# Kernel tuning notes

Measured on AMD Instinct MI355X. Metric: run time of the kernel, lower is better.

## Reference

```python
import jax, jax.numpy as jnp
import numpy as np

SPATIAL_SCALE = 0.125  # stride-8 FPN level
POINTS = 5


def _sample_points(bb):
    # bb: [N,H,W,5] = (cx, cy, w, h, theta) in image coords
    cx, cy, w, h, t = [bb[..., i] for i in range(5)]
    if POINTS == 1:
        px = cx[..., None]
        py = cy[..., None]
    else:
        vx = w * jnp.cos(t) * 0.5
        vy = w * jnp.sin(t) * 0.5
        wx = -h * jnp.sin(t) * 0.5
        wy = h * jnp.cos(t) * 0.5
        px = jnp.stack([cx, cx + vx + wx, cx - vx + wx, cx - vx - wx, cx + vx - wx], axis=-1)
        py = jnp.stack([cy, cy + vy + wy, cy - vy + wy, cy - vy - wy, cy + vy - wy], axis=-1)
    return px * SPATIAL_SCALE, py * SPATIAL_SCALE  # [N,H,W,P] feature-map coords


def _bilinear_gather(feat, y, x):
    # feat: [N,C,H,W]; y,x: [N,H,W,P] -> [N,H,W,P,C], mmcv-style bilinear w/ border rules
    N, C, H, W = feat.shape
    valid = (y >= -1.0) & (y <= H) & (x >= -1.0) & (x <= W)
    y = jnp.maximum(y, 0.0)
    x = jnp.maximum(x, 0.0)
    y_low = jnp.minimum(jnp.floor(y).astype(jnp.int32), H - 1)
    x_low = jnp.minimum(jnp.floor(x).astype(jnp.int32), W - 1)
    # if low index hits last row/col, snap coordinate onto it (ly/lx = 0)
    y = jnp.where(y_low >= H - 1, y_low.astype(feat.dtype), y)
    x = jnp.where(x_low >= W - 1, x_low.astype(feat.dtype), x)
    y_high = jnp.minimum(y_low + 1, H - 1)
    x_high = jnp.minimum(x_low + 1, W - 1)
    ly = y - y_low.astype(feat.dtype)
    lx = x - x_low.astype(feat.dtype)
    hy = 1.0 - ly
    hx = 1.0 - lx
    nn = jnp.arange(N)[:, None, None, None]  # broadcasts against [N,H,W,P]

    def g(yy, xx):
        return feat[nn, :, yy, xx]  # [N,H,W,P,C]

    val = ((hy * hx)[..., None] * g(y_low, x_low)
           + (hy * lx)[..., None] * g(y_low, x_high)
           + (ly * hx)[..., None] * g(y_high, x_low)
           + (ly * lx)[..., None] * g(y_high, x_high))
    return jnp.where(valid[..., None], val, 0.0)


def feature_refine(features, best_rbboxes):
    px, py = _sample_points(best_rbboxes)
    sampled = _bilinear_gather(features, py, px)       # [N,H,W,P,C]
    acc = sampled.sum(axis=3)                           # [N,H,W,C]
    return features + jnp.transpose(acc, (0, 3, 1, 2))  # [N,C,H,W]


def setup_inputs() -> dict:
    key = jax.random.key(0)
    k1, k2, k3, k4, k5, k6 = jax.random.split(key, 6)
    N, C, H, W = 4, 256, 128, 128
    IMG = 1024.0
    features = jax.random.normal(k1, (N, C, H, W), dtype=jnp.float32)
    cx = jax.random.uniform(k2, (N, H, W), minval=0.0, maxval=IMG)
    cy = jax.random.uniform(k3, (N, H, W), minval=0.0, maxval=IMG)
    bw = jax.random.uniform(k4, (N, H, W), minval=8.0, maxval=128.0)
    bh = jax.random.uniform(k5, (N, H, W), minval=8.0, maxval=128.0)
    th = jax.random.uniform(k6, (N, H, W), minval=-np.pi / 2, maxval=np.pi / 2)
    best_rbboxes = jnp.stack([cx, cy, bw, bh, th], axis=-1)  # [N,H,W,5]
    return {"features": features, "best_rbboxes": best_rbboxes}


def reference(features, best_rbboxes):
    return feature_refine(features, best_rbboxes)
```

## Files before the change

### kernel.cpp

```cpp
#include <hip/hip_runtime.h>


#define N_ 4
#define C_ 256
#define H_ 128
#define W_ 128
#define HW_ (H_ * W_)
#define SCALE 0.125f

typedef unsigned int uint32;

__device__ __forceinline__ uint32 f2bf(float f) {
    uint32 u = __float_as_uint(f);
    u = (u + 0x7FFF + ((u >> 16) & 1)) >> 16;
    return u;
}
__device__ __forceinline__ float blo(uint32 u) { return __uint_as_float(u << 16); }
__device__ __forceinline__ float bhi(uint32 u) { return __uint_as_float(u & 0xFFFF0000u); }

__global__ __launch_bounds__(1024, 8) void nchw2nhwc_geo(const float* __restrict__ in,
                                                         const float* __restrict__ bb,
                                                         uint32* __restrict__ outU,
                                                         uint32* __restrict__ geoG)
{
    __shared__ uint32 tile[64 * 260];
    const int t   = threadIdx.x;
    const int l   = t & 63;
    const int g   = t >> 6;
    const int hw0 = blockIdx.x * 256;
    const int ch  = blockIdx.y;
    const int n   = blockIdx.z;

    if (ch == 0 && t < 256) {
        const int px = n * HW_ + hw0 + t;
        const float* b = bb + (size_t)px * 5;
        const float cx = b[0], cy = b[1], bw = b[2], bh = b[3], th = b[4];
        const float st = sinf(th), ct = cosf(th);
        const float vx = bw * ct * 0.5f, vy = bw * st * 0.5f;
        const float wx = -bh * st * 0.5f, wy = bh * ct * 0.5f;
        const float pxs[5] = {cx, cx + vx + wx, cx - vx + wx, cx - vx - wx, cx + vx - wx};
        const float pys[5] = {cy, cy + vy + wy, cy - vy + wy, cy - vy - wy, cy + vy - wy};
        uint32* gw = geoG + (size_t)px * 32;
#pragma unroll
        for (int p = 0; p < 5; ++p) {
            float x = pxs[p] * SCALE;
            float y = pys[p] * SCALE;
            const bool valid = (y >= -1.0f) && (y <= (float)H_) &&
                               (x >= -1.0f) && (x <= (float)W_);
            y = fmaxf(y, 0.0f);
            x = fmaxf(x, 0.0f);
            int yl = min((int)y, H_ - 1);
            int xl = min((int)x, W_ - 1);
            if (yl >= H_ - 1) y = (float)yl;
            if (xl >= W_ - 1) x = (float)xl;
            const int yh = min(yl + 1, H_ - 1);
            const float ly = y - (float)yl, lx = x - (float)xl;
            const float hy = 1.0f - ly,     hx = 1.0f - lx;
            const int xa = min(xl, W_ - 2);
            float wA, wB;
            if (xl < W_ - 1) { wA = hx; wB = lx; }
            else             { wA = 0.0f; wB = 1.0f; }
            const float v = valid ? 1.0f : 0.0f;
            gw[p]      = (uint32)(yl * W_ + xa);
            gw[5 + p]  = (uint32)(yh * W_ + xa);
            gw[10 + p] = __float_as_uint(v * hy * wA);
            gw[15 + p] = __float_as_uint(v * hy * wB);
            gw[20 + p] = __float_as_uint(v * ly * wA);
            gw[25 + p] = __float_as_uint(v * ly * wB);
        }
        gw[30] = 0u; gw[31] = 0u;
    }

    const float* base = in + (size_t)n * C_ * HW_ + (size_t)(ch * 128) * HW_ + hw0 + 4 * l;
    float4 v0[4], v1[4];
#pragma unroll
    for (int r = 0; r < 4; ++r) {
        const int cp = g * 4 + r;
        v0[r] = *(const float4*)(base + (size_t)(2 * cp) * HW_);
        v1[r] = *(const float4*)(base + (size_t)(2 * cp + 1) * HW_);
    }
#pragma unroll
    for (int r = 0; r < 4; ++r) {
        const int cp = g * 4 + r;
        uint4 u;
        u.x = f2bf(v0[r].x) | (f2bf(v1[r].x) << 16);
        u.y = f2bf(v0[r].y) | (f2bf(v1[r].y) << 16);
        u.z = f2bf(v0[r].z) | (f2bf(v1[r].z) << 16);
        u.w = f2bf(v0[r].w) | (f2bf(v1[r].w) << 16);
        *(uint4*)&tile[cp * 260 + 4 * l] = u;
    }
    __syncthreads();
    uint32* dst = outU + ((size_t)n * HW_ + hw0) * 128 + ch * 64;
#pragma unroll
    for (int it = 0; it < 16; ++it) {
        const int f   = it * 1024 + t;
        const int row = f >> 6;
        const int q   = f & 63;
        dst[(size_t)row * 128 + q] = tile[q * 260 + row];
    }
}

__global__ __launch_bounds__(256, 8) void fr_refine(const uint32* __restrict__ nhwcU,
                                                    const uint32* __restrict__ geoG,
                                                    float* __restrict__ out)
{
    __shared__ float tile[32 * 128];
    const int t  = threadIdx.x;
    const int l  = t & 63;
    const int wv = __builtin_amdgcn_readfirstlane(t >> 6);
    const int bx = blockIdx.x;
    const int xcd = bx & 7;
    const int n   = xcd >> 1;
    const int ch  = xcd & 1;
    const int s   = bx >> 3;
    const int h   = s >> 2;
    const int w0  = (s & 3) * 32;

    const int chB = ch << 8;
    const int laneb = ((l & 15) << 4) + (((l >> 4) & 1) << 9);
    const bool hi = (l >= 32);
    const bool b4 = ((l >> 4) & 1) != 0;
    const int hwb = h * W_ + w0 + wv * 8;
    const uint32* gb = geoG + ((size_t)n * HW_ + hwb) * 32;
    const char* plane = (const char*)(nhwcU + (size_t)n * HW_ * 128);

#pragma unroll 1
    for (int p = 0; p < 8; ++p) {
        const uint32* g = gb + p * 32;

        int o0b[5], o1b[5];
        float w00[5], w01[5], w10[5], w11[5];
#pragma unroll
        for (int q = 0; q < 5; ++q) {
            o0b[q] = (int)__builtin_amdgcn_readfirstlane(g[q])     * 512 + chB;
            o1b[q] = (int)__builtin_amdgcn_readfirstlane(g[5 + q]) * 512 + chB;
            w00[q] = __uint_as_float(__builtin_amdgcn_readfirstlane(g[10 + q]));
            w01[q] = __uint_as_float(__builtin_amdgcn_readfirstlane(g[15 + q]));
            w10[q] = __uint_as_float(__builtin_amdgcn_readfirstlane(g[20 + q]));
            w11[q] = __uint_as_float(__builtin_amdgcn_readfirstlane(g[25 + q]));
        }

        uint4 rid = make_uint4(0u, 0u, 0u, 0u);
        if (l < 16)
            rid = *(const uint4*)(plane + (size_t)(hwb + p) * 512 + chB + ((l & 15) << 4));
        uint4 r[5];
#pragma unroll
        for (int q = 0; q < 5; ++q) {
            const int vof = (hi ? o1b[q] : o0b[q]) + laneb;
            r[q] = *(const uint4*)(plane + vof);
        }
        __builtin_amdgcn_sched_barrier(0);

        float a[8];
        a[0] = blo(rid.x); a[1] = bhi(rid.x);
        a[2] = blo(rid.y); a[3] = bhi(rid.y);
        a[4] = blo(rid.z); a[5] = bhi(rid.z);
        a[6] = blo(rid.w); a[7] = bhi(rid.w);
#pragma unroll
        for (int q = 0; q < 5; ++q) {
            const float wq = hi ? (b4 ? w11[q] : w10[q]) : (b4 ? w01[q] : w00[q]);
            a[0] = fmaf(wq, blo(r[q].x), a[0]); a[1] = fmaf(wq, bhi(r[q].x), a[1]);
            a[2] = fmaf(wq, blo(r[q].y), a[2]); a[3] = fmaf(wq, bhi(r[q].y), a[3]);
            a[4] = fmaf(wq, blo(r[q].z), a[4]); a[5] = fmaf(wq, bhi(r[q].z), a[5]);
            a[6] = fmaf(wq, blo(r[q].w), a[6]); a[7] = fmaf(wq, bhi(r[q].w), a[7]);
        }
#pragma unroll
        for (int k = 0; k < 8; ++k) {
            a[k] += __shfl_xor(a[k], 16, 64);
            a[k] += __shfl_xor(a[k], 32, 64);
        }
        if (l < 16) {
            const int px  = wv * 8 + p;
            const int swz = (px & 7) << 2;
            float* base = &tile[px * 128];
            *(float4*)&base[(l * 8) ^ swz]     = make_float4(a[0], a[1], a[2], a[3]);
            *(float4*)&base[(l * 8 + 4) ^ swz] = make_float4(a[4], a[5], a[6], a[7]);
        }
    }
    __syncthreads();
    const size_t obase = (size_t)n * C_ * HW_ + (size_t)(ch * 128) * HW_ + h * W_ + w0;
#pragma unroll
    for (int it = 0; it < 16; ++it) {
        const int flat = it * 256 + t;
        const int px = flat & 31;
        const int c  = flat >> 5;
        out[obase + (size_t)c * HW_ + px] = tile[px * 128 + (c ^ ((px & 7) << 2))];
    }
}

__global__ __launch_bounds__(256) void fr_kernel(
    const float* __restrict__ feat,
    const float* __restrict__ bb,
    float* __restrict__ out)
{
    const int lane = threadIdx.x & 63;
    const int wave = threadIdx.x >> 6;
    const int tile = blockIdx.x;
    const int wt   = tile & 1;
    const int h    = (tile >> 1) & (H_ - 1);
    const int n    = tile >> 8;
    const int w    = wt * 64 + lane;
    const int cb   = blockIdx.y;

    const float* b = bb + (size_t)((n * H_ + h) * W_ + w) * 5;
    const float cx = b[0], cy = b[1], bw = b[2], bh = b[3], th = b[4];
    const float st = sinf(th), ct = cosf(th);
    const float vx = bw * ct * 0.5f, vy = bw * st * 0.5f;
    const float wx = -bh * st * 0.5f, wy = bh * ct * 0.5f;
    const float pxs[5] = {cx, cx + vx + wx, cx - vx + wx, cx - vx - wx, cx + vx - wx};
    const float pys[5] = {cy, cy + vy + wy, cy - vy + wy, cy - vy - wy, cy + vy - wy};

    int   off0[5], off1[5];
    float wgt[20];
#pragma unroll
    for (int p = 0; p < 5; ++p) {
        float x = pxs[p] * SCALE;
        float y = pys[p] * SCALE;
        const bool valid = (y >= -1.0f) && (y <= (float)H_) &&
                           (x >= -1.0f) && (x <= (float)W_);
        y = fmaxf(y, 0.0f);
        x = fmaxf(x, 0.0f);
        int yl = min((int)y, H_ - 1);
        int xl = min((int)x, W_ - 1);
        if (yl >= H_ - 1) y = (float)yl;
        if (xl >= W_ - 1) x = (float)xl;
        const int yh = min(yl + 1, H_ - 1);
        const float ly = y - (float)yl, lx = x - (float)xl;
        const float hy = 1.0f - ly,     hx = 1.0f - lx;
        const int xa = min(xl, W_ - 2);
        float wA, wB;
        if (xl < W_ - 1) { wA = hx; wB = lx; }
        else             { wA = 0.0f; wB = 1.0f; }
        const float v = valid ? 1.0f : 0.0f;
        off0[p] = yl * W_ + xa;
        off1[p] = yh * W_ + xa;
        wgt[p * 4 + 0] = v * hy * wA;
        wgt[p * 4 + 1] = v * hy * wB;
        wgt[p * 4 + 2] = v * ly * wA;
        wgt[p * 4 + 3] = v * ly * wB;
    }

    const int hw = h * W_ + w;
    const size_t planeBase = ((size_t)n * C_ + cb * 64 + wave * 16) * HW_;
    const float* fp = feat + planeBase;
    float*       op = out  + planeBase;
    for (int it = 0; it < 16; ++it) {
        float acc = fp[hw];
#pragma unroll
        for (int p = 0; p < 5; ++p) {
            acc += wgt[p * 4 + 0] * fp[off0[p]]
                 + wgt[p * 4 + 1] * fp[off0[p] + 1]
                 + wgt[p * 4 + 2] * fp[off1[p]]
                 + wgt[p * 4 + 3] * fp[off1[p] + 1];
        }
        op[hw] = acc;
        fp += HW_;
        op += HW_;
    }
}

extern "C" void kernel_launch(void* const* d_in, const int* in_sizes, int n_in,
                              void* d_out, int out_size, void* d_ws, size_t ws_size,
                              hipStream_t stream) {
    const float* feat = (const float*)d_in[0];
    const float* bbox = (const float*)d_in[1];
    float* out = (float*)d_out;

    const size_t nhwcBytes = (size_t)N_ * HW_ * C_ * 2;
    const size_t geoBytes  = (size_t)N_ * HW_ * 32 * 4;
    if (ws_size >= nhwcBytes + geoBytes) {
        uint32* nhwcU = (uint32*)d_ws;
        uint32* geoG  = (uint32*)((char*)d_ws + nhwcBytes);
        nchw2nhwc_geo<<<dim3(HW_ / 256, 2, N_), dim3(1024), 0, stream>>>(feat, bbox, nhwcU, geoG);
        fr_refine<<<dim3(N_ * H_ * (W_ / 32) * 2), dim3(256), 0, stream>>>(nhwcU, geoG, out);
    } else {
        dim3 grid(N_ * H_ * (W_ / 64), C_ / 64, 1);
        fr_kernel<<<grid, dim3(256), 0, stream>>>(feat, bbox, out);
    }
}
```

Baseline: 158.6 us.

## Shrink transpose blocks, batch scalar geo loads, packed FMA, fp32 residual add

The transpose kernel now uses 512-thread blocks, each covering 128 pixels, with a smaller LDS tile, which gives more blocks and better occupancy. Gather offsets are pre-scaled to bytes in the geometry buffer. The refine kernel loads each pixel's 32-word geometry record with two s_load_dwordx16 instructions instead of many readfirstlane loads, and it accumulates with v_pk_fma_f32. The identity term is no longer a bf16 gather: fp32 features are read and added at the output store. That improves accuracy but adds an extra fp32 read of the full feature tensor.

```diff
diff --git a/kernel.cpp b/kernel.cpp
--- a/kernel.cpp
+++ b/kernel.cpp
@@ -9,6 +9,8 @@
 #define SCALE 0.125f
 
 typedef unsigned int uint32;
+typedef uint32 u32x16 __attribute__((ext_vector_type(16)));
+typedef float  f32x2  __attribute__((ext_vector_type(2)));
 
 __device__ __forceinline__ uint32 f2bf(float f) {
     uint32 u = __float_as_uint(f);
@@ -18,20 +20,22 @@
 __device__ __forceinline__ float blo(uint32 u) { return __uint_as_float(u << 16); }
 __device__ __forceinline__ float bhi(uint32 u) { return __uint_as_float(u & 0xFFFF0000u); }
 
-__global__ __launch_bounds__(1024, 8) void nchw2nhwc_geo(const float* __restrict__ in,
-                                                         const float* __restrict__ bb,
-                                                         uint32* __restrict__ outU,
-                                                         uint32* __restrict__ geoG)
+__global__ __launch_bounds__(512, 8) void nchw2nhwc_geo(const float* __restrict__ in,
+                                                        const float* __restrict__ bb,
+                                                        uint32* __restrict__ outU,
+                                                        uint32* __restrict__ geoG)
 {
-    __shared__ uint32 tile[64 * 260];
+    __shared__ uint32 tile[64 * 132];
     const int t   = threadIdx.x;
     const int l   = t & 63;
     const int g   = t >> 6;
-    const int hw0 = blockIdx.x * 256;
+    const int lw  = l & 31;
+    const int half = l >> 5;
+    const int hw0 = blockIdx.x * 128;
     const int ch  = blockIdx.y;
     const int n   = blockIdx.z;
 
-    if (ch == 0 && t < 256) {
+    if (ch == 0 && t < 128) {
         const int px = n * HW_ + hw0 + t;
         const float* b = bb + (size_t)px * 5;
         const float cx = b[0], cy = b[1], bw = b[2], bh = b[3], th = b[4];
@@ -61,8 +65,8 @@
             if (xl < W_ - 1) { wA = hx; wB = lx; }
             else             { wA = 0.0f; wB = 1.0f; }
             const float v = valid ? 1.0f : 0.0f;
-            gw[p]      = (uint32)(yl * W_ + xa);
-            gw[5 + p]  = (uint32)(yh * W_ + xa);
+            gw[p]      = (uint32)((yl * W_ + xa) * 512);
+            gw[5 + p]  = (uint32)((yh * W_ + xa) * 512);
             gw[10 + p] = __float_as_uint(v * hy * wA);
             gw[15 + p] = __float_as_uint(v * hy * wB);
             gw[20 + p] = __float_as_uint(v * ly * wA);
@@ -71,37 +75,38 @@
         gw[30] = 0u; gw[31] = 0u;
     }
 
-    const float* base = in + (size_t)n * C_ * HW_ + (size_t)(ch * 128) * HW_ + hw0 + 4 * l;
+    const float* base = in + (size_t)n * C_ * HW_ + (size_t)(ch * 128) * HW_ + hw0 + 4 * lw;
     float4 v0[4], v1[4];
 #pragma unroll
     for (int r = 0; r < 4; ++r) {
-        const int cp = g * 4 + r;
+        const int cp = g * 8 + half * 4 + r;
         v0[r] = *(const float4*)(base + (size_t)(2 * cp) * HW_);
         v1[r] = *(const float4*)(base + (size_t)(2 * cp + 1) * HW_);
     }
 #pragma unroll
     for (int r = 0; r < 4; ++r) {
-        const int cp = g * 4 + r;
+        const int cp = g * 8 + half * 4 + r;
         uint4 u;
         u.x = f2bf(v0[r].x) | (f2bf(v1[r].x) << 16);
         u.y = f2bf(v0[r].y) | (f2bf(v1[r].y) << 16);
         u.z = f2bf(v0[r].z) | (f2bf(v1[r].z) << 16);
         u.w = f2bf(v0[r].w) | (f2bf(v1[r].w) << 16);
-        *(uint4*)&tile[cp * 260 + 4 * l] = u;
+        *(uint4*)&tile[cp * 132 + 4 * lw] = u;
     }
     __syncthreads();
     uint32* dst = outU + ((size_t)n * HW_ + hw0) * 128 + ch * 64;
 #pragma unroll
     for (int it = 0; it < 16; ++it) {
-        const int f   = it * 1024 + t;
+        const int f   = it * 512 + t;
         const int row = f >> 6;
         const int q   = f & 63;
-        dst[(size_t)row * 128 + q] = tile[q * 260 + row];
+        dst[(size_t)row * 128 + q] = tile[q * 132 + row];
     }
 }
 
 __global__ __launch_bounds__(256, 8) void fr_refine(const uint32* __restrict__ nhwcU,
                                                     const uint32* __restrict__ geoG,
+                                                    const float* __restrict__ feat,
                                                     float* __restrict__ out)
 {
     __shared__ float tile[32 * 128];
@@ -116,65 +121,67 @@
     const int h   = s >> 2;
     const int w0  = (s & 3) * 32;
 
-    const int chB = ch << 8;
     const int laneb = ((l & 15) << 4) + (((l >> 4) & 1) << 9);
     const bool hi = (l >= 32);
     const bool b4 = ((l >> 4) & 1) != 0;
     const int hwb = h * W_ + w0 + wv * 8;
     const uint32* gb = geoG + ((size_t)n * HW_ + hwb) * 32;
-    const char* plane = (const char*)(nhwcU + (size_t)n * HW_ * 128);
+    const char* plane = (const char*)(nhwcU + (size_t)n * HW_ * 128) + (ch << 8);
 
 #pragma unroll 1
     for (int p = 0; p < 8; ++p) {
         const uint32* g = gb + p * 32;
 
-        int o0b[5], o1b[5];
-        float w00[5], w01[5], w10[5], w11[5];
+        u32x16 S0, S1;
+        asm volatile("s_load_dwordx16 %0, %2, 0x0\n"
+                     "s_load_dwordx16 %1, %2, 0x40\n"
+                     "s_waitcnt lgkmcnt(0)\n"
+                     : "=&s"(S0), "=&s"(S1)
+                     : "s"(g));
+        __builtin_amdgcn_sched_barrier(0);
+#define GW(i) ((i) < 16 ? S0[(i)] : S1[(i) - 16])
+
+        uint4 r[5];
+        f32x2 w2[5];
 #pragma unroll
         for (int q = 0; q < 5; ++q) {
-            o0b[q] = (int)__builtin_amdgcn_readfirstlane(g[q])     * 512 + chB;
-            o1b[q] = (int)__builtin_amdgcn_readfirstlane(g[5 + q]) * 512 + chB;
-            w00[q] = __uint_as_float(__builtin_amdgcn_readfirstlane(g[10 + q]));
-            w01[q] = __uint_as_float(__builtin_amdgcn_readfirstlane(g[15 + q]));
-            w10[q] = __uint_as_float(__builtin_amdgcn_readfirstlane(g[20 + q]));
-            w11[q] = __uint_as_float(__builtin_amdgcn_readfirstlane(g[25 + q]));
-        }
-
-        uint4 rid = make_uint4(0u, 0u, 0u, 0u);
-        if (l < 16)
-            rid = *(const uint4*)(plane + (size_t)(hwb + p) * 512 + chB + ((l & 15) << 4));
-        uint4 r[5];
+            const int vof = (int)(hi ? GW(5 + q) : GW(q)) + laneb;
+            r[q] = *(const uint4*)(plane + vof);
+            const float wq = __uint_as_float(hi ? (b4 ? GW(25 + q) : GW(20 + q))
+                                                : (b4 ? GW(15 + q) : GW(10 + q)));
+            w2[q].x = wq; w2[q].y = wq;
+        }
+        __builtin_amdgcn_sched_barrier(0);
+#undef GW
+
+        f32x2 acc[4];
+#pragma unroll
+        for (int k = 0; k < 4; ++k) { acc[k].x = 0.0f; acc[k].y = 0.0f; }
 #pragma unroll
         for (int q = 0; q < 5; ++q) {
-            const int vof = (hi ? o1b[q] : o0b[q]) + laneb;
-            r[q] = *(const uint4*)(plane + vof);
-        }
-        __builtin_amdgcn_sched_barrier(0);
-
-        float a[8];
-        a[0] = blo(rid.x); a[1] = bhi(rid.x);
-        a[2] = blo(rid.y); a[3] = bhi(rid.y);
-        a[4] = blo(rid.z); a[5] = bhi(rid.z);
-        a[6] = blo(rid.w); a[7] = bhi(rid.w);
-#pragma unroll
-        for (int q = 0; q < 5; ++q) {
-            const float wq = hi ? (b4 ? w11[q] : w10[q]) : (b4 ? w01[q] : w00[q]);
-            a[0] = fmaf(wq, blo(r[q].x), a[0]); a[1] = fmaf(wq, bhi(r[q].x), a[1]);
-            a[2] = fmaf(wq, blo(r[q].y), a[2]); a[3] = fmaf(wq, bhi(r[q].y), a[3]);
-            a[4] = fmaf(wq, blo(r[q].z), a[4]); a[5] = fmaf(wq, bhi(r[q].z), a[5]);
-            a[6] = fmaf(wq, blo(r[q].w), a[6]); a[7] = fmaf(wq, bhi(r[q].w), a[7]);
-        }
-#pragma unroll
-        for (int k = 0; k < 8; ++k) {
-            a[k] += __shfl_xor(a[k], 16, 64);
-            a[k] += __shfl_xor(a[k], 32, 64);
+            f32x2 u0, u1, u2, u3;
+            u0.x = blo(r[q].x); u0.y = bhi(r[q].x);
+            u1.x = blo(r[q].y); u1.y = bhi(r[q].y);
+            u2.x = blo(r[q].z); u2.y = bhi(r[q].z);
+            u3.x = blo(r[q].w); u3.y = bhi(r[q].w);
+            asm("v_pk_fma_f32 %0, %1, %2, %0" : "+v"(acc[0]) : "v"(u0), "v"(w2[q]));
+            asm("v_pk_fma_f32 %0, %1, %2, %0" : "+v"(acc[1]) : "v"(u1), "v"(w2[q]));
+            asm("v_pk_fma_f32 %0, %1, %2, %0" : "+v"(acc[2]) : "v"(u2), "v"(w2[q]));
+            asm("v_pk_fma_f32 %0, %1, %2, %0" : "+v"(acc[3]) : "v"(u3), "v"(w2[q]));
+        }
+#pragma unroll
+        for (int k = 0; k < 4; ++k) {
+            acc[k].x += __shfl_xor(acc[k].x, 16, 64);
+            acc[k].y += __shfl_xor(acc[k].y, 16, 64);
+            acc[k].x += __shfl_xor(acc[k].x, 32, 64);
+            acc[k].y += __shfl_xor(acc[k].y, 32, 64);
         }
         if (l < 16) {
             const int px  = wv * 8 + p;
             const int swz = (px & 7) << 2;
             float* base = &tile[px * 128];
-            *(float4*)&base[(l * 8) ^ swz]     = make_float4(a[0], a[1], a[2], a[3]);
-            *(float4*)&base[(l * 8 + 4) ^ swz] = make_float4(a[4], a[5], a[6], a[7]);
+            *(float4*)&base[(l * 8) ^ swz]     = make_float4(acc[0].x, acc[0].y, acc[1].x, acc[1].y);
+            *(float4*)&base[(l * 8 + 4) ^ swz] = make_float4(acc[2].x, acc[2].y, acc[3].x, acc[3].y);
         }
     }
     __syncthreads();
@@ -184,7 +191,8 @@
         const int flat = it * 256 + t;
         const int px = flat & 31;
         const int c  = flat >> 5;
-        out[obase + (size_t)c * HW_ + px] = tile[px * 128 + (c ^ ((px & 7) << 2))];
+        const size_t idx = obase + (size_t)c * HW_ + px;
+        out[idx] = feat[idx] + tile[px * 128 + (c ^ ((px & 7) << 2))];
     }
 }
 
@@ -271,8 +279,8 @@
     if (ws_size >= nhwcBytes + geoBytes) {
         uint32* nhwcU = (uint32*)d_ws;
         uint32* geoG  = (uint32*)((char*)d_ws + nhwcBytes);
-        nchw2nhwc_geo<<<dim3(HW_ / 256, 2, N_), dim3(1024), 0, stream>>>(feat, bbox, nhwcU, geoG);
-        fr_refine<<<dim3(N_ * H_ * (W_ / 32) * 2), dim3(256), 0, stream>>>(nhwcU, geoG, out);
+        nchw2nhwc_geo<<<dim3(HW_ / 128, 2, N_), dim3(512), 0, stream>>>(feat, bbox, nhwcU, geoG);
+        fr_refine<<<dim3(N_ * H_ * (W_ / 32) * 2), dim3(256), 0, stream>>>(nhwcU, geoG, feat, out);
     } else {
         dim3 grid(N_ * H_ * (W_ / 64), C_ / 64, 1);
         fr_kernel<<<grid, dim3(256), 0, stream>>>(feat, bbox, out);
```

Result: slower. 192.2 us (+21.2%).
